# Kernel optimization log

Hardware: AMD Instinct MI355X
Metric: run time of the kernel (lower is better)

## Reference

```python
import jax, jax.numpy as jnp
import numpy as np

D = 512
H = 8
DH = D // H
FF = 2 * D
EPS = 1e-5


def _layernorm(x, g, b):
    mu = jnp.mean(x, axis=-1, keepdims=True)
    var = jnp.mean(jnp.square(x - mu), axis=-1, keepdims=True)
    return (x - mu) * jax.lax.rsqrt(var + EPS) * g + b


def setup_inputs() -> dict:
    key = jax.random.key(0)
    ks = jax.random.split(key, 8)
    s = 0.02
    x = jax.random.normal(ks[0], (1, 4096, D), dtype=jnp.float32)
    w_qkv = jax.random.normal(ks[1], (D, 3 * D), dtype=jnp.float32) * s
    b_qkv = jnp.zeros((3 * D,), jnp.float32)
    w_out = jax.random.normal(ks[2], (D, D), dtype=jnp.float32) * s
    b_out = jnp.zeros((D,), jnp.float32)
    w_ff1 = jax.random.normal(ks[3], (D, FF), dtype=jnp.float32) * s
    b_ff1 = jnp.zeros((FF,), jnp.float32)
    w_ff2 = jax.random.normal(ks[4], (FF, D), dtype=jnp.float32) * s
    b_ff2 = jnp.zeros((D,), jnp.float32)
    g1 = jnp.ones((D,), jnp.float32)
    bt1 = jnp.zeros((D,), jnp.float32)
    g2 = jnp.ones((D,), jnp.float32)
    bt2 = jnp.zeros((D,), jnp.float32)
    return {"x": x, "w_qkv": w_qkv, "b_qkv": b_qkv, "w_out": w_out, "b_out": b_out,
            "w_ff1": w_ff1, "b_ff1": b_ff1, "w_ff2": w_ff2, "b_ff2": b_ff2,
            "g1": g1, "bt1": bt1, "g2": g2, "bt2": bt2}


def reference(x, w_qkv, b_qkv, w_out, b_out, w_ff1, b_ff1, w_ff2, b_ff2, g1, bt1, g2, bt2):
    B, S, _ = x.shape
    h = _layernorm(x, g1, bt1)
    qkv = h @ w_qkv + b_qkv                      # [B,S,3D]
    qkv = qkv.reshape(B, S, 3, H, DH)
    q, k, v = qkv[:, :, 0], qkv[:, :, 1], qkv[:, :, 2]   # [B,S,H,DH]
    scores = jnp.einsum('bqhd,bkhd->bhqk', q, k) / np.sqrt(DH).astype(np.float32)
    causal = jnp.tril(jnp.ones((S, S), dtype=bool))
    scores = jnp.where(causal, scores, -jnp.inf)
    attn = jax.nn.softmax(scores, axis=-1)
    out = jnp.einsum('bhqk,bkhd->bqhd', attn, v).reshape(B, S, D)
    x = x + out @ w_out + b_out
    h2 = _layernorm(x, g2, bt2)
    ff = jax.nn.gelu(h2 @ w_ff1 + b_ff1, approximate=False) @ w_ff2 + b_ff2
    return x + ff
```

## Files before the change

kernel.cpp:

```cpp
#include <hip/hip_runtime.h>
#include <math.h>

#define D 512
#define H 8
#define DH 64
#define S 4096
#define FF 1024

typedef __attribute__((ext_vector_type(8))) short bf16x8;
typedef __attribute__((ext_vector_type(4))) float f32x4;
typedef __attribute__((ext_vector_type(16))) float f32x16;

__device__ __forceinline__ unsigned short f2bf(float f) {
    union { float f; unsigned u; } c; c.f = f;
    unsigned r = (c.u + 0x7fff + ((c.u >> 16) & 1)) >> 16;
    return (unsigned short)r;
}
__device__ __forceinline__ float bf2f(unsigned short u) {
    union { unsigned u; float f; } c; c.u = ((unsigned)u) << 16;
    return c.f;
}
__device__ __forceinline__ unsigned asu(float f) {
    union { float f; unsigned u; } c; c.f = f; return c.u;
}

__global__ __launch_bounds__(256) void transpose_all(const float* __restrict__ wqkv,
                                                     const float* __restrict__ wout,
                                                     const float* __restrict__ wff1,
                                                     const float* __restrict__ wff2,
                                                     unsigned short* __restrict__ oqkv,
                                                     unsigned short* __restrict__ oout,
                                                     unsigned short* __restrict__ off1,
                                                     unsigned short* __restrict__ off2) {
    __shared__ unsigned short tile[32][33];
    int id = blockIdx.x;
    const float* src; unsigned short* dst; int K, N, lid;
    if (id < 768)       { src = wqkv; dst = oqkv; K = 512;  N = 1536; lid = id; }
    else if (id < 1024) { src = wout; dst = oout; K = 512;  N = 512;  lid = id - 768; }
    else if (id < 1536) { src = wff1; dst = off1; K = 512;  N = 1024; lid = id - 1024; }
    else                { src = wff2; dst = off2; K = 1024; N = 512;  lid = id - 1536; }
    int nb = N / 32;
    int n0 = (lid % nb) * 32, k0 = (lid / nb) * 32;
    int tx = threadIdx.x & 31, ty = threadIdx.x >> 5;
#pragma unroll
    for (int i = 0; i < 32; i += 8)
        tile[ty + i][tx] = f2bf(src[(size_t)(k0 + ty + i) * N + n0 + tx]);
    __syncthreads();
#pragma unroll
    for (int i = 0; i < 32; i += 8)
        dst[(size_t)(n0 + ty + i) * K + k0 + tx] = tile[tx][ty + i];
}

__global__ __launch_bounds__(256) void transpose_v(const unsigned short* __restrict__ qkv,
                                                   unsigned short* __restrict__ vT) {
    __shared__ unsigned short tile[32][33];
    int s0 = blockIdx.x * 32, d0 = blockIdx.y * 32;
    int tx = threadIdx.x & 31, ty = threadIdx.x >> 5;
#pragma unroll
    for (int i = 0; i < 32; i += 8)
        tile[ty + i][tx] = qkv[(size_t)(s0 + ty + i) * (3 * D) + 2 * D + d0 + tx];
    __syncthreads();
#pragma unroll
    for (int i = 0; i < 32; i += 8)
        vT[(size_t)(d0 + ty + i) * S + s0 + tx] = tile[tx][ty + i];
}

__global__ __launch_bounds__(256) void ln_kernel(const float* __restrict__ x,
                                                 const float* __restrict__ g,
                                                 const float* __restrict__ bta,
                                                 unsigned short* __restrict__ out) {
    int row = blockIdx.x, tid = threadIdx.x;
    const float* xr = x + (size_t)row * D;
    float2 v = *(const float2*)(xr + tid * 2);
    float s = v.x + v.y;
    float sq = v.x * v.x + v.y * v.y;
#pragma unroll
    for (int m = 1; m < 64; m <<= 1) { s += __shfl_xor(s, m); sq += __shfl_xor(sq, m); }
    __shared__ float red[8];
    int wave = tid >> 6, lane = tid & 63;
    if (lane == 0) { red[wave] = s; red[4 + wave] = sq; }
    __syncthreads();
    s = red[0] + red[1] + red[2] + red[3];
    sq = red[4] + red[5] + red[6] + red[7];
    float mu = s * (1.f / D);
    float var = sq * (1.f / D) - mu * mu;
    float rstd = rsqrtf(var + 1e-5f);
    int i = tid * 2;
    float2 gg = *(const float2*)(g + i);
    float2 bb = *(const float2*)(bta + i);
    out[(size_t)row * D + i]     = f2bf((v.x - mu) * rstd * gg.x + bb.x);
    out[(size_t)row * D + i + 1] = f2bf((v.y - mu) * rstd * gg.y + bb.y);
}

#define BM 128
#define BN 128
#define BK 32
#define LDT 40

enum { EPI_BF16 = 0, EPI_RESID_F32 = 1, EPI_GELU_BF16 = 2 };

template <int EPI>
__global__ __launch_bounds__(256, 2) void gemm_kernel(const unsigned short* __restrict__ A,
                                                      const unsigned short* __restrict__ BT,
                                                      const float* __restrict__ bias,
                                                      const float* __restrict__ resid,
                                                      void* __restrict__ out,
                                                      int M, int N, int K) {
    __shared__ __align__(16) unsigned short sA[BM * LDT];
    __shared__ __align__(16) unsigned short sB[BN * LDT];
    int tid = threadIdx.x;
    int wave = tid >> 6, lane = tid & 63;
    int quad = lane >> 4, l16 = lane & 15;
    int wr = (wave >> 1) * 64, wc = (wave & 1) * 64;
    int m0 = blockIdx.y * BM, n0 = blockIdx.x * BN;

    f32x4 acc[4][4];
#pragma unroll
    for (int i = 0; i < 4; i++)
#pragma unroll
        for (int j = 0; j < 4; j++) acc[i][j] = (f32x4){0.f, 0.f, 0.f, 0.f};

    int ar = tid >> 2;
    int ac = (tid & 3) * 8;
    const unsigned short* Ap = A + (size_t)(m0 + ar) * K + ac;
    const unsigned short* Ap2 = Ap + (size_t)64 * K;
    const unsigned short* Bp = BT + (size_t)(n0 + ar) * K + ac;
    const unsigned short* Bp2 = Bp + (size_t)64 * K;
    unsigned short* sAw = sA + ar * LDT + ac;
    unsigned short* sAw2 = sA + (ar + 64) * LDT + ac;
    unsigned short* sBw = sB + ar * LDT + ac;
    unsigned short* sBw2 = sB + (ar + 64) * LDT + ac;

    for (int k0 = 0; k0 < K; k0 += BK) {
        bf16x8 a0 = *(const bf16x8*)(Ap + k0);
        bf16x8 a1 = *(const bf16x8*)(Ap2 + k0);
        bf16x8 b0 = *(const bf16x8*)(Bp + k0);
        bf16x8 b1 = *(const bf16x8*)(Bp2 + k0);
        __syncthreads();
        *(bf16x8*)sAw = a0;
        *(bf16x8*)sAw2 = a1;
        *(bf16x8*)sBw = b0;
        *(bf16x8*)sBw2 = b1;
        __syncthreads();
        bf16x8 af[4], bfr[4];
#pragma unroll
        for (int i = 0; i < 4; i++)
            af[i] = *(const bf16x8*)(sA + (wr + i * 16 + l16) * LDT + quad * 8);
#pragma unroll
        for (int i = 0; i < 4; i++)
            bfr[i] = *(const bf16x8*)(sB + (wc + i * 16 + l16) * LDT + quad * 8);
#pragma unroll
        for (int mi = 0; mi < 4; mi++)
#pragma unroll
            for (int ni = 0; ni < 4; ni++)
                acc[mi][ni] = __builtin_amdgcn_mfma_f32_16x16x32_bf16(af[mi], bfr[ni], acc[mi][ni], 0, 0, 0);
    }

#pragma unroll
    for (int mi = 0; mi < 4; mi++)
#pragma unroll
        for (int ni = 0; ni < 4; ni++)
#pragma unroll
            for (int r = 0; r < 4; r++) {
                int row = m0 + wr + mi * 16 + quad * 4 + r;
                int col = n0 + wc + ni * 16 + l16;
                float v = acc[mi][ni][r] + bias[col];
                size_t idx = (size_t)row * N + col;
                if constexpr (EPI == EPI_RESID_F32) {
                    ((float*)out)[idx] = v + resid[idx];
                } else if constexpr (EPI == EPI_GELU_BF16) {
                    v = 0.5f * v * (1.f + erff(v * 0.70710678118f));
                    ((unsigned short*)out)[idx] = f2bf(v);
                } else {
                    ((unsigned short*)out)[idx] = f2bf(v);
                }
            }
}

#define LDF 72
#define LDO 68

__global__ __launch_bounds__(256, 3) void flash4_kernel(const unsigned short* __restrict__ qkv,
                                                        const unsigned short* __restrict__ vT,
                                                        unsigned short* __restrict__ O_part,
                                                        float* __restrict__ l_part) {
    __shared__ __align__(16) unsigned short sK[2][64 * LDF];
    __shared__ __align__(16) unsigned short sV[2][64 * LDF];

    int tid = threadIdx.x;
    int w = tid >> 6, lane = tid & 63;
    int lq = lane & 31, hb = lane >> 5;

    int h = blockIdx.x & 7;
    int u = blockIdx.x >> 3;
    int Q = 31, c = 0, acc = 0;
    for (int qq = 31; qq >= 0; --qq) {
        int n = (2 * qq + 17) >> 4;
        if (u < acc + n) { Q = qq; c = u - acc; break; }
        acc += n;
    }
    int T = 2 * Q + 2;
    int t0c = c * 16;
    int t1c = min(t0c + 16, T);
    int q0w = Q * 128 + w * 32;
    int qrow = q0w + lq;
    int qmax = q0w + 31;

    const float CEXP = 0.18033688f;

    bf16x8 qf[4];
#pragma unroll
    for (int dc = 0; dc < 4; dc++) {
        bf16x8 qraw = *(const bf16x8*)(qkv + (size_t)qrow * (3 * D) + h * DH + dc * 16 + hb * 8);
        bf16x8 qs;
#pragma unroll
        for (int j = 0; j < 8; j++)
            qs[j] = (short)f2bf(bf2f((unsigned short)qraw[j]) * CEXP);
        qf[dc] = qs;
    }

    f32x16 oa[2];
#pragma unroll
    for (int i = 0; i < 16; i++) { oa[0][i] = 0.f; oa[1][i] = 0.f; }
    float lsum = 0.f;

    int rr = tid >> 3;
    int cc8 = (tid & 7) * 8;
    const unsigned short* kgb = qkv + (size_t)rr * (3 * D) + D + h * DH + cc8;
    const unsigned short* vgb = vT + (size_t)(h * DH + rr) * S + cc8;

    bf16x8 gk0, gk1, gv0, gv1;
    auto glb = [&](int t) {
        const unsigned short* kg = kgb + (size_t)t * 64 * (3 * D);
        gk0 = *(const bf16x8*)(kg);
        gk1 = *(const bf16x8*)(kg + (size_t)32 * (3 * D));
        const unsigned short* vg = vgb + t * 64;
        gv0 = *(const bf16x8*)(vg);
        gv1 = *(const bf16x8*)(vg + (size_t)32 * S);
    };

    glb(t0c);
    for (int t = t0c; t < t1c; ++t) {
        int buf = (t - t0c) & 1;
        unsigned short* dk = &sK[buf][rr * LDF + cc8];
        *(bf16x8*)dk = gk0;
        *(bf16x8*)(dk + 32 * LDF) = gk1;
        unsigned short* dv = &sV[buf][rr * LDF + cc8];
        *(bf16x8*)dv = gv0;
        *(bf16x8*)(dv + 32 * LDF) = gv1;
        if (t + 1 < t1c) glb(t + 1);
        __syncthreads();

        if (64 * t > qmax) continue;

        f32x16 sa[2];
#pragma unroll
        for (int i = 0; i < 16; i++) { sa[0][i] = 0.f; sa[1][i] = 0.f; }
#pragma unroll
        for (int kt = 0; kt < 2; kt++)
#pragma unroll
            for (int dc = 0; dc < 4; dc++) {
                bf16x8 kf = *(const bf16x8*)(&sK[buf][(kt * 32 + lq) * LDF + dc * 16 + hb * 8]);
                sa[kt] = __builtin_amdgcn_mfma_f32_32x32x16_bf16(kf, qf[dc], sa[kt], 0, 0, 0);
            }

        bool dmask = (64 * t + 63 > qmax);
        unsigned p2[2][8];
#pragma unroll
        for (int kt = 0; kt < 2; kt++) {
            float e[16];
#pragma unroll
            for (int r = 0; r < 16; r++) {
                float v = __builtin_amdgcn_exp2f(sa[kt][r]);
                if (dmask) {
                    int key = 64 * t + kt * 32 + (r & 3) + 8 * (r >> 2) + 4 * hb;
                    if (key > qrow) v = 0.f;
                }
                e[r] = v;
                lsum += v;
            }
#pragma unroll
            for (int rr2 = 0; rr2 < 8; rr2++)
                p2[kt][rr2] = __builtin_amdgcn_perm(asu(e[2 * rr2 + 1]) + 0x8000u,
                                                    asu(e[2 * rr2]) + 0x8000u, 0x07060302u);
        }

#pragma unroll
        for (int kc = 0; kc < 4; kc++) {
            int kt = kc >> 1;
            int b0i = (kc & 1) * 4;
            unsigned a0 = p2[kt][b0i + 0], a1 = p2[kt][b0i + 1];
            unsigned b0 = p2[kt][b0i + 2], b1 = p2[kt][b0i + 3];
            unsigned s0 = hb ? a0 : b0, s1 = hb ? a1 : b1;
            unsigned x0 = __shfl_xor(s0, 32), x1 = __shfl_xor(s1, 32);
            unsigned l0 = hb ? b0 : a0, l1 = hb ? b1 : a1;
            union { unsigned u[4]; bf16x8 v; } fr;
            fr.u[0] = hb ? x0 : l0;
            fr.u[1] = hb ? x1 : l1;
            fr.u[2] = hb ? l0 : x0;
            fr.u[3] = hb ? l1 : x1;
#pragma unroll
            for (int dt = 0; dt < 2; dt++) {
                bf16x8 vf = *(const bf16x8*)(&sV[buf][(dt * 32 + lq) * LDF + kc * 16 + hb * 8]);
                oa[dt] = __builtin_amdgcn_mfma_f32_32x32x16_bf16(vf, fr.v, oa[dt], 0, 0, 0);
            }
        }
    }

    lsum += __shfl_xor(lsum, 32);
    if (hb == 0)
        l_part[((size_t)c * H + h) * S + q0w + lq] = lsum;

    __syncthreads();
    unsigned short* sOw = (unsigned short*)sK + w * 32 * LDO;
#pragma unroll
    for (int kt = 0; kt < 2; kt++)
#pragma unroll
        for (int r = 0; r < 16; r++) {
            int d = kt * 32 + (r & 3) + 8 * (r >> 2) + 4 * hb;
            sOw[lq * LDO + d] = f2bf(oa[kt][r]);
        }
    asm volatile("s_waitcnt lgkmcnt(0)" ::: "memory");
    unsigned short* Op = O_part + ((size_t)c * S + q0w) * D + h * DH;
#pragma unroll
    for (int it = 0; it < 4; it++) {
        int rq = (lane >> 3) + it * 8;
        bf16x8 val = *(const bf16x8*)(sOw + rq * LDO + (lane & 7) * 8);
        *(bf16x8*)(Op + (size_t)rq * D + (lane & 7) * 8) = val;
    }
}

__global__ __launch_bounds__(256) void norm_kernel(const unsigned short* __restrict__ O_part,
                                                   const float* __restrict__ l_part,
                                                   unsigned short* __restrict__ O) {
    int idx = blockIdx.x * 256 + threadIdx.x;
    int row = idx >> 9, col = idx & 511;
    int h = col >> 6;
    int nch = (2 * (row >> 7) + 17) >> 4;
    float o = 0.f, l = 0.f;
    for (int cc = 0; cc < nch; cc++) {
        o += bf2f(O_part[((size_t)cc * S + row) * D + col]);
        l += l_part[((size_t)cc * H + h) * S + row];
    }
    O[idx] = f2bf(o / l);
}

extern "C" void kernel_launch(void* const* d_in, const int* in_sizes, int n_in,
                              void* d_out, int out_size, void* d_ws, size_t ws_size,
                              hipStream_t stream) {
    const float* x     = (const float*)d_in[0];
    const float* w_qkv = (const float*)d_in[1];
    const float* b_qkv = (const float*)d_in[2];
    const float* w_out = (const float*)d_in[3];
    const float* b_out = (const float*)d_in[4];
    const float* w_ff1 = (const float*)d_in[5];
    const float* b_ff1 = (const float*)d_in[6];
    const float* w_ff2 = (const float*)d_in[7];
    const float* b_ff2 = (const float*)d_in[8];
    const float* g1    = (const float*)d_in[9];
    const float* bt1   = (const float*)d_in[10];
    const float* g2    = (const float*)d_in[11];
    const float* bt2   = (const float*)d_in[12];

    char* ws = (char*)d_ws;
    size_t off = 0;
    auto alloc = [&](size_t bytes) {
        void* p = ws + off;
        off += (bytes + 255) & ~(size_t)255;
        return p;
    };
    unsigned short* hbuf   = (unsigned short*)alloc((size_t)S * D * 2);
    unsigned short* qkvbuf = (unsigned short*)alloc((size_t)S * 3 * D * 2);
    unsigned short* vTbuf  = (unsigned short*)alloc((size_t)D * S * 2);
    unsigned short* Obuf   = (unsigned short*)alloc((size_t)S * D * 2);
    unsigned short* wqkvT  = (unsigned short*)alloc((size_t)3 * D * D * 2);
    unsigned short* woutT  = (unsigned short*)alloc((size_t)D * D * 2);
    unsigned short* wff1T  = (unsigned short*)alloc((size_t)FF * D * 2);
    unsigned short* wff2T  = (unsigned short*)alloc((size_t)D * FF * 2);
    unsigned short* Opart  = (unsigned short*)alloc((size_t)4 * S * D * 2);
    float*          lpart  = (float*)alloc((size_t)4 * H * S * 4);
    unsigned short* h2buf  = hbuf;
    unsigned short* ff1buf = qkvbuf;
    float*          x2buf  = (float*)Opart;

    transpose_all<<<dim3(2048), 256, 0, stream>>>(w_qkv, w_out, w_ff1, w_ff2,
                                                  wqkvT, woutT, wff1T, wff2T);

    ln_kernel<<<S, 256, 0, stream>>>(x, g1, bt1, hbuf);
    gemm_kernel<EPI_BF16><<<dim3(3 * D / BN, S / BM), 256, 0, stream>>>(
        hbuf, wqkvT, b_qkv, nullptr, qkvbuf, S, 3 * D, D);
    transpose_v<<<dim3(S / 32, D / 32), 256, 0, stream>>>(qkvbuf, vTbuf);
    flash4_kernel<<<dim3(640), 256, 0, stream>>>(qkvbuf, vTbuf, Opart, lpart);
    norm_kernel<<<dim3(S * D / 256), 256, 0, stream>>>(Opart, lpart, Obuf);
    gemm_kernel<EPI_RESID_F32><<<dim3(D / BN, S / BM), 256, 0, stream>>>(
        Obuf, woutT, b_out, x, x2buf, S, D, D);
    ln_kernel<<<S, 256, 0, stream>>>(x2buf, g2, bt2, h2buf);
    gemm_kernel<EPI_GELU_BF16><<<dim3(FF / BN, S / BM), 256, 0, stream>>>(
        h2buf, wff1T, b_ff1, nullptr, ff1buf, S, FF, D);
    gemm_kernel<EPI_RESID_F32><<<dim3(D / BN, S / BM), 256, 0, stream>>>(
        ff1buf, wff2T, b_ff2, x2buf, (float*)d_out, S, D, FF);
}
```

Measured before the change: 215.2 us.

## Rewrite GEMMs with direct global-to-LDS loads, swizzle, and finer attention split

```diff
diff --git a/kernel.cpp b/kernel.cpp
--- a/kernel.cpp
+++ b/kernel.cpp
@@ -20,8 +20,11 @@
     union { unsigned u; float f; } c; c.u = ((unsigned)u) << 16;
     return c.f;
 }
-__device__ __forceinline__ unsigned asu(float f) {
-    union { float f; unsigned u; } c; c.f = f; return c.u;
+
+__device__ __forceinline__ void gl_lds16(const void* g, void* l) {
+    __builtin_amdgcn_global_load_lds(
+        (const __attribute__((address_space(1))) void*)g,
+        (__attribute__((address_space(3))) void*)l, 16, 0, 0);
 }
 
 __global__ __launch_bounds__(256) void transpose_all(const float* __restrict__ wqkv,
@@ -92,79 +95,82 @@
     out[(size_t)row * D + i + 1] = f2bf((v.y - mu) * rstd * gg.y + bb.y);
 }
 
-#define BM 128
-#define BN 128
-#define BK 32
-#define LDT 40
-
 enum { EPI_BF16 = 0, EPI_RESID_F32 = 1, EPI_GELU_BF16 = 2 };
 
-template <int EPI>
-__global__ __launch_bounds__(256, 2) void gemm_kernel(const unsigned short* __restrict__ A,
-                                                      const unsigned short* __restrict__ BT,
-                                                      const float* __restrict__ bias,
-                                                      const float* __restrict__ resid,
-                                                      void* __restrict__ out,
-                                                      int M, int N, int K) {
-    __shared__ __align__(16) unsigned short sA[BM * LDT];
-    __shared__ __align__(16) unsigned short sB[BN * LDT];
+template <int EPI, int WMI>
+__global__ __launch_bounds__(256, WMI == 4 ? 3 : 4)
+void gemm2_kernel(const unsigned short* __restrict__ A,
+                  const unsigned short* __restrict__ BT,
+                  const float* __restrict__ bias,
+                  const float* __restrict__ resid,
+                  void* __restrict__ out,
+                  int M, int N, int K) {
+    constexpr int BM = 32 * WMI;
+    constexpr int BN = 128;
+    constexpr int APH = BM * 8 / 256;
+    __shared__ __align__(16) unsigned short sA[BM * 64];
+    __shared__ __align__(16) unsigned short sB[BN * 64];
+
     int tid = threadIdx.x;
     int wave = tid >> 6, lane = tid & 63;
     int quad = lane >> 4, l16 = lane & 15;
-    int wr = (wave >> 1) * 64, wc = (wave & 1) * 64;
+    int lx = l16 & 7;
+    int wr = (wave >> 1) * (BM / 2), wc = (wave & 1) * 64;
     int m0 = blockIdx.y * BM, n0 = blockIdx.x * BN;
 
-    f32x4 acc[4][4];
-#pragma unroll
-    for (int i = 0; i < 4; i++)
+    f32x4 acc[WMI][4];
+#pragma unroll
+    for (int i = 0; i < WMI; i++)
 #pragma unroll
         for (int j = 0; j < 4; j++) acc[i][j] = (f32x4){0.f, 0.f, 0.f, 0.f};
 
-    int ar = tid >> 2;
-    int ac = (tid & 3) * 8;
-    const unsigned short* Ap = A + (size_t)(m0 + ar) * K + ac;
-    const unsigned short* Ap2 = Ap + (size_t)64 * K;
-    const unsigned short* Bp = BT + (size_t)(n0 + ar) * K + ac;
-    const unsigned short* Bp2 = Bp + (size_t)64 * K;
-    unsigned short* sAw = sA + ar * LDT + ac;
-    unsigned short* sAw2 = sA + (ar + 64) * LDT + ac;
-    unsigned short* sBw = sB + ar * LDT + ac;
-    unsigned short* sBw2 = sB + (ar + 64) * LDT + ac;
-
-    for (int k0 = 0; k0 < K; k0 += BK) {
-        bf16x8 a0 = *(const bf16x8*)(Ap + k0);
-        bf16x8 a1 = *(const bf16x8*)(Ap2 + k0);
-        bf16x8 b0 = *(const bf16x8*)(Bp + k0);
-        bf16x8 b1 = *(const bf16x8*)(Bp2 + k0);
+    int srow = tid >> 3;
+    int spc = tid & 7;
+    int scc = spc ^ (srow & 7);
+    const unsigned short* Abase = A + (size_t)(m0 + srow) * K + scc * 8;
+    const unsigned short* Bbase = BT + (size_t)(n0 + srow) * K + scc * 8;
+    unsigned short* sAdst = sA + (tid & ~63) * 8;
+    unsigned short* sBdst = sB + (tid & ~63) * 8;
+
+    for (int k0 = 0; k0 < K; k0 += 64) {
         __syncthreads();
-        *(bf16x8*)sAw = a0;
-        *(bf16x8*)sAw2 = a1;
-        *(bf16x8*)sBw = b0;
-        *(bf16x8*)sBw2 = b1;
+#pragma unroll
+        for (int ph = 0; ph < APH; ph++)
+            gl_lds16(Abase + (size_t)(ph * 32) * K + k0, sAdst + ph * 256 * 8);
+#pragma unroll
+        for (int ph = 0; ph < 4; ph++)
+            gl_lds16(Bbase + (size_t)(ph * 32) * K + k0, sBdst + ph * 256 * 8);
+        asm volatile("s_waitcnt vmcnt(0)" ::: "memory");
         __syncthreads();
-        bf16x8 af[4], bfr[4];
-#pragma unroll
-        for (int i = 0; i < 4; i++)
-            af[i] = *(const bf16x8*)(sA + (wr + i * 16 + l16) * LDT + quad * 8);
-#pragma unroll
-        for (int i = 0; i < 4; i++)
-            bfr[i] = *(const bf16x8*)(sB + (wc + i * 16 + l16) * LDT + quad * 8);
-#pragma unroll
-        for (int mi = 0; mi < 4; mi++)
+
+#pragma unroll
+        for (int ks = 0; ks < 2; ks++) {
+            int cxs = ((ks * 4 + quad) ^ lx) * 8;
+            bf16x8 af[WMI], bfr[4];
+#pragma unroll
+            for (int mi = 0; mi < WMI; mi++)
+                af[mi] = *(const bf16x8*)(sA + (wr + mi * 16 + l16) * 64 + (cxs ^ (0)));
 #pragma unroll
             for (int ni = 0; ni < 4; ni++)
-                acc[mi][ni] = __builtin_amdgcn_mfma_f32_16x16x32_bf16(af[mi], bfr[ni], acc[mi][ni], 0, 0, 0);
+                bfr[ni] = *(const bf16x8*)(sB + (wc + ni * 16 + l16) * 64 + cxs);
+#pragma unroll
+            for (int mi = 0; mi < WMI; mi++)
+#pragma unroll
+                for (int ni = 0; ni < 4; ni++)
+                    acc[mi][ni] = __builtin_amdgcn_mfma_f32_16x16x32_bf16(af[mi], bfr[ni], acc[mi][ni], 0, 0, 0);
+        }
     }
 
 #pragma unroll
-    for (int mi = 0; mi < 4; mi++)
-#pragma unroll
-        for (int ni = 0; ni < 4; ni++)
+    for (int mi = 0; mi < WMI; mi++)
+#pragma unroll
+        for (int ni = 0; ni < 4; ni++) {
+            int col = n0 + wc + ni * 16 + l16;
+            float bs = bias[col];
 #pragma unroll
             for (int r = 0; r < 4; r++) {
                 int row = m0 + wr + mi * 16 + quad * 4 + r;
-                int col = n0 + wc + ni * 16 + l16;
-                float v = acc[mi][ni][r] + bias[col];
+                float v = acc[mi][ni][r] + bs;
                 size_t idx = (size_t)row * N + col;
                 if constexpr (EPI == EPI_RESID_F32) {
                     ((float*)out)[idx] = v + resid[idx];
@@ -175,12 +181,13 @@
                     ((unsigned short*)out)[idx] = f2bf(v);
                 }
             }
+        }
 }
 
 #define LDF 72
 #define LDO 68
 
-__global__ __launch_bounds__(256, 3) void flash4_kernel(const unsigned short* __restrict__ qkv,
+__global__ __launch_bounds__(256, 4) void flash5_kernel(const unsigned short* __restrict__ qkv,
                                                         const unsigned short* __restrict__ vT,
                                                         unsigned short* __restrict__ O_part,
                                                         float* __restrict__ l_part) {
@@ -195,13 +202,13 @@
     int u = blockIdx.x >> 3;
     int Q = 31, c = 0, acc = 0;
     for (int qq = 31; qq >= 0; --qq) {
-        int n = (2 * qq + 17) >> 4;
+        int n = (qq >> 2) + 1;
         if (u < acc + n) { Q = qq; c = u - acc; break; }
         acc += n;
     }
     int T = 2 * Q + 2;
-    int t0c = c * 16;
-    int t1c = min(t0c + 16, T);
+    int t0c = c * 8;
+    int t1c = min(t0c + 8, T);
     int q0w = Q * 128 + w * 32;
     int qrow = q0w + lq;
     int qmax = q0w + 31;
@@ -210,14 +217,8 @@
 
     bf16x8 qf[4];
 #pragma unroll
-    for (int dc = 0; dc < 4; dc++) {
-        bf16x8 qraw = *(const bf16x8*)(qkv + (size_t)qrow * (3 * D) + h * DH + dc * 16 + hb * 8);
-        bf16x8 qs;
-#pragma unroll
-        for (int j = 0; j < 8; j++)
-            qs[j] = (short)f2bf(bf2f((unsigned short)qraw[j]) * CEXP);
-        qf[dc] = qs;
-    }
+    for (int dc = 0; dc < 4; dc++)
+        qf[dc] = *(const bf16x8*)(qkv + (size_t)qrow * (3 * D) + h * DH + dc * 16 + hb * 8);
 
     f32x16 oa[2];
 #pragma unroll
@@ -271,7 +272,7 @@
             float e[16];
 #pragma unroll
             for (int r = 0; r < 16; r++) {
-                float v = __builtin_amdgcn_exp2f(sa[kt][r]);
+                float v = __builtin_amdgcn_exp2f(sa[kt][r] * CEXP);
                 if (dmask) {
                     int key = 64 * t + kt * 32 + (r & 3) + 8 * (r >> 2) + 4 * hb;
                     if (key > qrow) v = 0.f;
@@ -281,8 +282,7 @@
             }
 #pragma unroll
             for (int rr2 = 0; rr2 < 8; rr2++)
-                p2[kt][rr2] = __builtin_amdgcn_perm(asu(e[2 * rr2 + 1]) + 0x8000u,
-                                                    asu(e[2 * rr2]) + 0x8000u, 0x07060302u);
+                p2[kt][rr2] = ((unsigned)f2bf(e[2 * rr2 + 1]) << 16) | f2bf(e[2 * rr2]);
         }
 
 #pragma unroll
@@ -336,7 +336,7 @@
     int idx = blockIdx.x * 256 + threadIdx.x;
     int row = idx >> 9, col = idx & 511;
     int h = col >> 6;
-    int nch = (2 * (row >> 7) + 17) >> 4;
+    int nch = ((row >> 7) >> 2) + 1;
     float o = 0.f, l = 0.f;
     for (int cc = 0; cc < nch; cc++) {
         o += bf2f(O_part[((size_t)cc * S + row) * D + col]);
@@ -377,8 +377,8 @@
     unsigned short* woutT  = (unsigned short*)alloc((size_t)D * D * 2);
     unsigned short* wff1T  = (unsigned short*)alloc((size_t)FF * D * 2);
     unsigned short* wff2T  = (unsigned short*)alloc((size_t)D * FF * 2);
-    unsigned short* Opart  = (unsigned short*)alloc((size_t)4 * S * D * 2);
-    float*          lpart  = (float*)alloc((size_t)4 * H * S * 4);
+    unsigned short* Opart  = (unsigned short*)alloc((size_t)8 * S * D * 2);
+    float*          lpart  = (float*)alloc((size_t)8 * H * S * 4);
     unsigned short* h2buf  = hbuf;
     unsigned short* ff1buf = qkvbuf;
     float*          x2buf  = (float*)Opart;
@@ -387,16 +387,16 @@
                                                   wqkvT, woutT, wff1T, wff2T);
 
     ln_kernel<<<S, 256, 0, stream>>>(x, g1, bt1, hbuf);
-    gemm_kernel<EPI_BF16><<<dim3(3 * D / BN, S / BM), 256, 0, stream>>>(
+    gemm2_kernel<EPI_BF16, 4><<<dim3(12, 32), 256, 0, stream>>>(
         hbuf, wqkvT, b_qkv, nullptr, qkvbuf, S, 3 * D, D);
     transpose_v<<<dim3(S / 32, D / 32), 256, 0, stream>>>(qkvbuf, vTbuf);
-    flash4_kernel<<<dim3(640), 256, 0, stream>>>(qkvbuf, vTbuf, Opart, lpart);
+    flash5_kernel<<<dim3(1152), 256, 0, stream>>>(qkvbuf, vTbuf, Opart, lpart);
     norm_kernel<<<dim3(S * D / 256), 256, 0, stream>>>(Opart, lpart, Obuf);
-    gemm_kernel<EPI_RESID_F32><<<dim3(D / BN, S / BM), 256, 0, stream>>>(
+    gemm2_kernel<EPI_RESID_F32, 2><<<dim3(4, 64), 256, 0, stream>>>(
         Obuf, woutT, b_out, x, x2buf, S, D, D);
     ln_kernel<<<S, 256, 0, stream>>>(x2buf, g2, bt2, h2buf);
-    gemm_kernel<EPI_GELU_BF16><<<dim3(FF / BN, S / BM), 256, 0, stream>>>(
+    gemm2_kernel<EPI_GELU_BF16, 4><<<dim3(8, 32), 256, 0, stream>>>(
         h2buf, wff1T, b_ff1, nullptr, ff1buf, S, FF, D);
-    gemm_kernel<EPI_RESID_F32><<<dim3(D / BN, S / BM), 256, 0, stream>>>(
+    gemm2_kernel<EPI_RESID_F32, 2><<<dim3(4, 64), 256, 0, stream>>>(
         ff1buf, wff2T, b_ff2, x2buf, (float*)d_out, S, D, FF);
 }
```

New measurement: 205.7 us. 1.05x faster.
